# Performance work log

Hardware: AMD Instinct MI355X
Metric: run time of the kernel (lower is better)

Reference implementation:

```python
import jax, jax.numpy as jnp
import numpy as np
from jax import lax

DIM = 48
HEADS = 8
NBLK = 4
DN = ('NCHW', 'OIHW', 'NCHW')
EPS = 1e-12  # F.normalize clamp_min


def _to_blocks(t, b, heads, c, h1, w1, N):
    # 'b (head c) (h1 N_h) (w1 N_w) -> b head (c N_h N_w) (h1 w1)'
    t = t.reshape(b, heads, c, h1, N, w1, N)
    t = t.transpose(0, 1, 2, 4, 6, 3, 5)  # b head c N_h N_w h1 w1
    return t.reshape(b, heads, c * N * N, h1 * w1)


def _from_blocks(t, b, heads, c, h1, w1, N):
    t = t.reshape(b, heads, c, N, N, h1, w1)
    t = t.transpose(0, 1, 2, 5, 3, 6, 4)  # b head c h1 N_h w1 N_w
    return t.reshape(b, heads * c, h1 * N, w1 * N)


def setup_inputs() -> dict:
    key = jax.random.key(0)
    ks = jax.random.split(key, 5)
    return {
        'x': jax.random.normal(ks[0], (2, DIM, 512, 512), dtype=jnp.float32),
        'qkv_w': jax.random.normal(ks[1], (3 * DIM, DIM, 1, 1), dtype=jnp.float32) * 0.05,
        'dw_w': jax.random.normal(ks[2], (3 * DIM, 1, 3, 3), dtype=jnp.float32) * 0.05,
        'proj_w': jax.random.normal(ks[3], (DIM, DIM, 1, 1), dtype=jnp.float32) * 0.05,
        'temperature': jnp.ones((HEADS, 1, 1), dtype=jnp.float32),
    }


def reference(x, qkv_w, dw_w, proj_w, temperature):
    b, _, h, w = x.shape
    N = NBLK
    h_pad = (-h) % N
    w_pad = (-w) % N
    if h_pad or w_pad:
        x = jnp.pad(x, ((0, 0), (0, 0), (0, h_pad), (0, w_pad)), mode='reflect')
    h_after, w_after = h + h_pad, w + w_pad
    h1, w1 = h_after // N, w_after // N

    # 1x1 pointwise conv then 3x3 depthwise conv
    qkv = lax.conv_general_dilated(x, qkv_w, (1, 1), 'VALID', dimension_numbers=DN)
    qkv = lax.conv_general_dilated(qkv, dw_w, (1, 1), ((1, 1), (1, 1)),
                                   dimension_numbers=DN, feature_group_count=3 * DIM)
    q, k, v = jnp.split(qkv, 3, axis=1)

    c = DIM // HEADS
    q = _to_blocks(q, b, HEADS, c, h1, w1, N)  # [b, head, c*N*N, h1*w1]
    k = _to_blocks(k, b, HEADS, c, h1, w1, N)
    v = _to_blocks(v, b, HEADS, c, h1, w1, N)

    q = q / jnp.maximum(jnp.linalg.norm(q, axis=-1, keepdims=True), EPS)
    k = k / jnp.maximum(jnp.linalg.norm(k, axis=-1, keepdims=True), EPS)

    attn = jnp.einsum('bhcn,bhdn->bhcd', q, k) * temperature  # [b, head, cb, cb]
    attn = jax.nn.softmax(attn, axis=-1)
    out = jnp.einsum('bhcd,bhdn->bhcn', attn, v)

    out = _from_blocks(out, b, HEADS, c, h1, w1, N)  # [b, dim, h_after, w_after]
    out = lax.conv_general_dilated(out, proj_w, (1, 1), 'VALID', dimension_numbers=DN)
    return out[:, :, :h, :w]
```

## Files before the change

### kernel.cpp

```cpp
#include <hip/hip_runtime.h>
#include <cstddef>

#define S 512
#define SHIFT_HW 18
#define NCOL 16384

#define QB_OFF 0ull
#define KB_OFF 25165824ull
#define VB_OFF 50331648ull
#define G_OFF  75497472ull
#define SQ_OFF 75644928ull
#define SK_OFF 75646464ull
#define A_OFF  75648000ull

#define QS_STRIDE 327

__global__ __launch_bounds__(384, 4) void k1_qkv_dw(
    const float* __restrict__ x, const float* __restrict__ qkv_w,
    const float* __restrict__ dw_w,
    float* __restrict__ qb, float* __restrict__ kb, float* __restrict__ vb)
{
  const int t = threadIdx.x;
  const int b = blockIdx.z;
  const int W0 = blockIdx.x * 16, H0 = blockIdx.y * 16;
  __shared__ float qs[24 * QS_STRIDE];
  __shared__ float dws[1296];
  __shared__ float qws[2][1152];

  for (int i = t; i < 1296; i += 384) dws[i] = dw_w[i];
  for (int i = t; i < 288; i += 384)
    ((float4*)qws[0])[i] = ((const float4*)qkv_w)[i];

  float xv[48];
  const int p  = t;
  const int hy = p / 18, hx = p % 18;
  const int Hg = H0 - 1 + hy, Wg = W0 - 1 + hx;
  const bool inb = (t < 324) && (Hg >= 0) && (Hg < S) && (Wg >= 0) && (Wg < S);
  const float* xb = x + ((size_t)b * 48 << SHIFT_HW) + (inb ? ((Hg << 9) + Wg) : 0);
  #pragma unroll
  for (int ic = 0; ic < 48; ++ic) {
    float v = 0.0f;
    if (inb) v = xb[(size_t)ic << SHIFT_HW];
    xv[ic] = v;
  }

  const int ch = t >> 4;
  const int y  = t & 15;
  const int nb = (blockIdx.y * 4 + (y >> 2)) * 128 + blockIdx.x * 4;
  const float* qrow = qs + ch * QS_STRIDE + y * 18;

  __syncthreads();

  #pragma unroll 1
  for (int g = 0; g < 6; ++g) {
    if (t < 324) {
      const float* wgp = qws[g & 1];
      #pragma unroll
      for (int oc = 0; oc < 24; oc += 2) {
        float a0 = 0.f, a1 = 0.f;
        #pragma unroll
        for (int ic4 = 0; ic4 < 12; ++ic4) {
          const float4 w0 = *(const float4*)(wgp + oc * 48 + ic4 * 4);
          const float4 w1 = *(const float4*)(wgp + (oc + 1) * 48 + ic4 * 4);
          a0 += w0.x * xv[ic4 * 4 + 0] + w0.y * xv[ic4 * 4 + 1]
              + w0.z * xv[ic4 * 4 + 2] + w0.w * xv[ic4 * 4 + 3];
          a1 += w1.x * xv[ic4 * 4 + 0] + w1.y * xv[ic4 * 4 + 1]
              + w1.z * xv[ic4 * 4 + 2] + w1.w * xv[ic4 * 4 + 3];
        }
        qs[oc * QS_STRIDE + p]       = a0;
        qs[(oc + 1) * QS_STRIDE + p] = a1;
      }
    } else if (g < 5) {
      float4* dstq = (float4*)qws[(g + 1) & 1];
      const float4* srcq = (const float4*)qkv_w + (g + 1) * 288;
      for (int i = t - 324; i < 288; i += 60) dstq[i] = srcq[i];
    }
    __syncthreads();

    const int tensor = g >> 1;
    const int chbase = (g & 1) * 24;
    const int chg  = chbase + ch;
    const int head = chg / 6, c = chg - 6 * head;
    float* dst = (tensor == 0) ? qb : (tensor == 1) ? kb : vb;
    float* dstp = dst + (size_t)((b * 8 + head) * 16384 + nb) * 96
                      + c * 16 + (y & 3) * 4;
    const float* wp = dws + (tensor * 48 + chg) * 9;
    const float w0 = wp[0], w1 = wp[1], w2 = wp[2];
    const float w3 = wp[3], w4 = wp[4], w5 = wp[5];
    const float w6 = wp[6], w7 = wp[7], w8 = wp[8];

    float p00 = qrow[0], p01 = qrow[18], p02 = qrow[36];
    float p10 = qrow[1], p11 = qrow[19], p12 = qrow[37];
    #pragma unroll
    for (int wl = 0; wl < 4; ++wl) {
      float o[4];
      #pragma unroll
      for (int u = 0; u < 4; ++u) {
        const int xq = wl * 4 + u;
        const float n0 = qrow[xq + 2];
        const float n1 = qrow[xq + 20];
        const float n2 = qrow[xq + 38];
        o[u] = w0 * p00 + w1 * p10 + w2 * n0
             + w3 * p01 + w4 * p11 + w5 * n1
             + w6 * p02 + w7 * p12 + w8 * n2;
        p00 = p10; p01 = p11; p02 = p12;
        p10 = n0;  p11 = n1;  p12 = n2;
      }
      float4 v4 = {o[0], o[1], o[2], o[3]};
      *(float4*)(dstp + (size_t)wl * 96) = v4;
    }
    __syncthreads();
  }
}

__global__ __launch_bounds__(256, 3) void k3_gram(
    const float* __restrict__ qb, const float* __restrict__ kb,
    float* __restrict__ G, float* __restrict__ sq, float* __restrict__ sk)
{
  const int t  = threadIdx.x;
  const int bh = blockIdx.y;
  const int n0 = blockIdx.x * 256;
  __shared__ float qt[6144];
  __shared__ float kt[6144];
  const int ti = t >> 4, tj = t & 15;
  float acc[6][6];
  #pragma unroll
  for (int r = 0; r < 6; ++r)
    #pragma unroll
    for (int s_ = 0; s_ < 6; ++s_) acc[r][s_] = 0.f;
  float ss = 0.f;
  const float* qbase = qb + (size_t)bh * 16384 * 96;
  const float* kbase = kb + (size_t)bh * 16384 * 96;

  #pragma unroll 1
  for (int st = 0; st < 4; ++st) {
    __syncthreads();
    const float4* qsrc = (const float4*)(qbase + (size_t)(n0 + st * 64) * 96);
    const float4* ksrc = (const float4*)(kbase + (size_t)(n0 + st * 64) * 96);
    #pragma unroll
    for (int r = 0; r < 6; ++r) {
      const int f4 = r * 256 + t;
      ((float4*)qt)[f4] = qsrc[f4];
      ((float4*)kt)[f4] = ksrc[f4];
    }
    __syncthreads();
    #pragma unroll 2
    for (int nn = 0; nn < 64; ++nn) {
      const float* qr = qt + nn * 96 + ti * 6;
      const float* kr = kt + nn * 96 + tj * 6;
      const float2 q0 = *(const float2*)(qr);
      const float2 q1 = *(const float2*)(qr + 2);
      const float2 q2 = *(const float2*)(qr + 4);
      const float2 k0 = *(const float2*)(kr);
      const float2 k1 = *(const float2*)(kr + 2);
      const float2 k2 = *(const float2*)(kr + 4);
      const float qv[6] = {q0.x, q0.y, q1.x, q1.y, q2.x, q2.y};
      const float kv[6] = {k0.x, k0.y, k1.x, k1.y, k2.x, k2.y};
      #pragma unroll
      for (int r = 0; r < 6; ++r)
        #pragma unroll
        for (int s_ = 0; s_ < 6; ++s_)
          acc[r][s_] += qv[r] * kv[s_];
    }
    if (t < 192) {
      const float* base = (t < 96) ? qt : kt;
      const int srow = (t < 96) ? t : (t - 96);
      float s2 = 0.f;
      #pragma unroll 8
      for (int nn = 0; nn < 64; ++nn) {
        const float v = base[nn * 96 + srow];
        s2 += v * v;
      }
      ss += s2;
    }
  }
  float* Gb = G + (size_t)bh * 9216;
  #pragma unroll
  for (int r = 0; r < 6; ++r)
    #pragma unroll
    for (int s_ = 0; s_ < 6; ++s_)
      atomicAdd(Gb + (ti * 6 + r) * 96 + (tj * 6 + s_), acc[r][s_]);
  if (t < 96)       atomicAdd(sq + bh * 96 + t,        ss);
  else if (t < 192) atomicAdd(sk + bh * 96 + (t - 96), ss);
}

__global__ __launch_bounds__(128) void k4_softmax(
    const float* __restrict__ G, const float* __restrict__ sq,
    const float* __restrict__ sk, const float* __restrict__ temp,
    float* __restrict__ A)
{
  const int i  = blockIdx.x;
  const int bh = blockIdx.y;
  const int h  = bh & 7;
  const int t  = threadIdx.x;
  __shared__ float red[128];

  const float nq    = fmaxf(sqrtf(sq[bh * 96 + i]), 1e-12f);
  const float scale = temp[h] / nq;
  float logit = 0.f, val = -1e30f;
  if (t < 96) {
    const float nk = fmaxf(sqrtf(sk[bh * 96 + t]), 1e-12f);
    logit = G[(size_t)bh * 9216 + i * 96 + t] * scale / nk;
    val = logit;
  }
  red[t] = val; __syncthreads();
  #pragma unroll
  for (int o = 64; o > 0; o >>= 1) {
    if (t < o) red[t] = fmaxf(red[t], red[t + o]);
    __syncthreads();
  }
  const float m = red[0]; __syncthreads();
  const float e = (t < 96) ? __expf(logit - m) : 0.f;
  red[t] = e; __syncthreads();
  #pragma unroll
  for (int o = 64; o > 0; o >>= 1) {
    if (t < o) red[t] += red[t + o];
    __syncthreads();
  }
  const float ssum = red[0];
  if (t < 96) A[(size_t)bh * 9216 + i * 96 + t] = e / ssum;
}

__global__ __launch_bounds__(256, 3) void k5_av_proj(
    const float* __restrict__ vb, const float* __restrict__ A,
    const float* __restrict__ pw, float* __restrict__ out)
{
  const int t  = threadIdx.x;
  const int wg = blockIdx.x, hh = blockIdx.y, b = blockIdx.z;
  const int n0 = hh * 128 + wg * 16;
  __shared__ float smem[12288];

  #pragma unroll
  for (int it = 0; it < 12; ++it) {
    const int i4  = it * 256 + t;
    const int h   = i4 / 384;
    const int q   = i4 - h * 384;
    const int r4g = q >> 6;
    const int rem = q & 63;
    const int nl  = rem >> 2;
    const int r4  = r4g * 4 + (rem & 3);
    const float4 v = *(const float4*)(vb
        + (size_t)((b * 8 + h) * 16384 + n0 + nl) * 96 + r4 * 4);
    float* dl = smem + (h * 96 + r4 * 4) * 16 + nl;
    dl[0] = v.x; dl[16] = v.y; dl[32] = v.z; dl[48] = v.w;
  }
  __syncthreads();

  float4 res[6][2];
  #pragma unroll 1
  for (int r = 0; r < 6; ++r) {
    const int task = r * 256 + t;
    const int n4 = task & 3;
    const int ip = (task >> 2) % 48;
    const int h  = task / 192;
    const int i0 = ip * 2;
    const float* arow0 = A + (size_t)((b * 8 + h) * 96 + i0) * 96;
    const float* arow1 = arow0 + 96;
    const float* vp = smem + h * 1536 + n4 * 4;
    float4 a0 = {0, 0, 0, 0}, a1 = {0, 0, 0, 0};
    #pragma unroll 2
    for (int j4 = 0; j4 < 24; ++j4) {
      const float4 w0 = *(const float4*)(arow0 + j4 * 4);
      const float4 w1 = *(const float4*)(arow1 + j4 * 4);
      const float4 v0 = *(const float4*)(vp + (j4 * 4 + 0) * 16);
      const float4 v1 = *(const float4*)(vp + (j4 * 4 + 1) * 16);
      const float4 v2 = *(const float4*)(vp + (j4 * 4 + 2) * 16);
      const float4 v3 = *(const float4*)(vp + (j4 * 4 + 3) * 16);
      a0.x += w0.x * v0.x + w0.y * v1.x + w0.z * v2.x + w0.w * v3.x;
      a0.y += w0.x * v0.y + w0.y * v1.y + w0.z * v2.y + w0.w * v3.y;
      a0.z += w0.x * v0.z + w0.y * v1.z + w0.z * v2.z + w0.w * v3.z;
      a0.w += w0.x * v0.w + w0.y * v1.w + w0.z * v2.w + w0.w * v3.w;
      a1.x += w1.x * v0.x + w1.y * v1.x + w1.z * v2.x + w1.w * v3.x;
      a1.y += w1.x * v0.y + w1.y * v1.y + w1.z * v2.y + w1.w * v3.y;
      a1.z += w1.x * v0.z + w1.y * v1.z + w1.z * v2.z + w1.w * v3.z;
      a1.w += w1.x * v0.w + w1.y * v1.w + w1.z * v2.w + w1.w * v3.w;
    }
    res[r][0] = a0; res[r][1] = a1;
  }
  __syncthreads();

  #pragma unroll
  for (int r = 0; r < 6; ++r) {
    const int task = r * 256 + t;
    const int n4 = task & 3;
    const int ip = (task >> 2) % 48;
    const int h  = task / 192;
    const int i0 = ip * 2, i1 = i0 + 1;
    *(float4*)(smem + ((h * 6 + (i0 >> 4)) * 16 + (i0 & 15)) * 16 + n4 * 4) = res[r][0];
    *(float4*)(smem + ((h * 6 + (i1 >> 4)) * 16 + (i1 & 15)) * 16 + n4 * 4) = res[r][1];
  }
  __syncthreads();

  const int xl = t & 63, ph = t >> 6;
  const int p  = ph * 4 + (xl & 3);
  const int wwl = xl >> 2;
  float sv[48];
  #pragma unroll
  for (int ic = 0; ic < 48; ++ic) sv[ic] = smem[(ic * 16 + p) * 16 + wwl];
  const int H = hh * 4 + ph;
  const int Wp = wg * 64 + xl;
  float* outp = out + ((size_t)b * 48 << SHIFT_HW) + (H << 9) + Wp;
  #pragma unroll 1
  for (int oc = 0; oc < 48; oc += 2) {
    float acc0 = 0.f, acc1 = 0.f;
    #pragma unroll
    for (int ic = 0; ic < 48; ++ic) {
      acc0 += pw[oc * 48 + ic]       * sv[ic];
      acc1 += pw[(oc + 1) * 48 + ic] * sv[ic];
    }
    outp[(size_t)oc << SHIFT_HW]       = acc0;
    outp[(size_t)(oc + 1) << SHIFT_HW] = acc1;
  }
}

extern "C" void kernel_launch(void* const* d_in, const int* in_sizes, int n_in,
                              void* d_out, int out_size, void* d_ws, size_t ws_size,
                              hipStream_t stream) {
  const float* x      = (const float*)d_in[0];
  const float* qkv_w  = (const float*)d_in[1];
  const float* dw_w   = (const float*)d_in[2];
  const float* proj_w = (const float*)d_in[3];
  const float* temp   = (const float*)d_in[4];
  float* ws = (float*)d_ws;
  float* qb = ws + QB_OFF;
  float* kb = ws + KB_OFF;
  float* vb = ws + VB_OFF;
  float* G  = ws + G_OFF;
  float* sq = ws + SQ_OFF;
  float* sk = ws + SK_OFF;
  float* A  = ws + A_OFF;

  hipMemsetAsync(G, 0, (size_t)(147456 + 3072) * sizeof(float), stream);

  k1_qkv_dw<<<dim3(32, 32, 2), 384, 0, stream>>>(x, qkv_w, dw_w, qb, kb, vb);
  k3_gram<<<dim3(64, 16), 256, 0, stream>>>(qb, kb, G, sq, sk);
  k4_softmax<<<dim3(96, 16), 128, 0, stream>>>(G, sq, sk, temp, A);
  k5_av_proj<<<dim3(8, 128, 2), 256, 0, stream>>>(vb, A, proj_w, (float*)d_out);
}
```

Measured before the change: 874.0 us.

## Restage qkv weights via registers, write partial Grams, retile AV/proj kernel

k1 now uses a single qkv weight buffer. The next group's weights are loaded into registers during the depthwise stage and stored to shared memory afterwards, and occupancy and the smem stride are changed. k3 handles twice as many columns per block and writes per-block partial Gram matrices into the output buffer instead of using atomics, and k4 sums those 32 partials. k5 moves to 384 threads with an XCD-aware block index mapping, gives each thread full rows for the AV product, and adds a rotated smem layout to reduce bank conflicts. This trades atomic contention and the G memset for extra partial-sum reads in the softmax kernel.

```diff
diff --git a/kernel.cpp b/kernel.cpp
--- a/kernel.cpp
+++ b/kernel.cpp
@@ -8,14 +8,13 @@
 #define QB_OFF 0ull
 #define KB_OFF 25165824ull
 #define VB_OFF 50331648ull
-#define G_OFF  75497472ull
 #define SQ_OFF 75644928ull
 #define SK_OFF 75646464ull
 #define A_OFF  75648000ull
 
-#define QS_STRIDE 327
-
-__global__ __launch_bounds__(384, 4) void k1_qkv_dw(
+#define QS_STRIDE 324
+
+__global__ __launch_bounds__(384, 6) void k1_qkv_dw(
     const float* __restrict__ x, const float* __restrict__ qkv_w,
     const float* __restrict__ dw_w,
     float* __restrict__ qb, float* __restrict__ kb, float* __restrict__ vb)
@@ -25,11 +24,11 @@
   const int W0 = blockIdx.x * 16, H0 = blockIdx.y * 16;
   __shared__ float qs[24 * QS_STRIDE];
   __shared__ float dws[1296];
-  __shared__ float qws[2][1152];
+  __shared__ float qws[1152];
 
   for (int i = t; i < 1296; i += 384) dws[i] = dw_w[i];
   for (int i = t; i < 288; i += 384)
-    ((float4*)qws[0])[i] = ((const float4*)qkv_w)[i];
+    ((float4*)qws)[i] = ((const float4*)qkv_w)[i];
 
   float xv[48];
   const int p  = t;
@@ -54,7 +53,7 @@
   #pragma unroll 1
   for (int g = 0; g < 6; ++g) {
     if (t < 324) {
-      const float* wgp = qws[g & 1];
+      const float* wgp = qws;
       #pragma unroll
       for (int oc = 0; oc < 24; oc += 2) {
         float a0 = 0.f, a1 = 0.f;
@@ -70,12 +69,12 @@
         qs[oc * QS_STRIDE + p]       = a0;
         qs[(oc + 1) * QS_STRIDE + p] = a1;
       }
-    } else if (g < 5) {
-      float4* dstq = (float4*)qws[(g + 1) & 1];
-      const float4* srcq = (const float4*)qkv_w + (g + 1) * 288;
-      for (int i = t - 324; i < 288; i += 60) dstq[i] = srcq[i];
-    }
-    __syncthreads();
+    }
+    __syncthreads();
+
+    float4 stg;
+    const bool do_stage = (g < 5) && (t < 288);
+    if (do_stage) stg = *((const float4*)qkv_w + (g + 1) * 288 + t);
 
     const int tensor = g >> 1;
     const int chbase = (g & 1) * 24;
@@ -109,17 +108,19 @@
       float4 v4 = {o[0], o[1], o[2], o[3]};
       *(float4*)(dstp + (size_t)wl * 96) = v4;
     }
+
+    if (do_stage) ((float4*)qws)[t] = stg;
     __syncthreads();
   }
 }
 
 __global__ __launch_bounds__(256, 3) void k3_gram(
     const float* __restrict__ qb, const float* __restrict__ kb,
-    float* __restrict__ G, float* __restrict__ sq, float* __restrict__ sk)
+    float* __restrict__ Gp, float* __restrict__ sq, float* __restrict__ sk)
 {
   const int t  = threadIdx.x;
   const int bh = blockIdx.y;
-  const int n0 = blockIdx.x * 256;
+  const int n0 = blockIdx.x * 512;
   __shared__ float qt[6144];
   __shared__ float kt[6144];
   const int ti = t >> 4, tj = t & 15;
@@ -133,7 +134,7 @@
   const float* kbase = kb + (size_t)bh * 16384 * 96;
 
   #pragma unroll 1
-  for (int st = 0; st < 4; ++st) {
+  for (int st = 0; st < 8; ++st) {
     __syncthreads();
     const float4* qsrc = (const float4*)(qbase + (size_t)(n0 + st * 64) * 96);
     const float4* ksrc = (const float4*)(kbase + (size_t)(n0 + st * 64) * 96);
@@ -174,18 +175,18 @@
       ss += s2;
     }
   }
-  float* Gb = G + (size_t)bh * 9216;
+  float* Gb = Gp + (size_t)(blockIdx.x * 16 + bh) * 9216;
   #pragma unroll
   for (int r = 0; r < 6; ++r)
     #pragma unroll
     for (int s_ = 0; s_ < 6; ++s_)
-      atomicAdd(Gb + (ti * 6 + r) * 96 + (tj * 6 + s_), acc[r][s_]);
+      Gb[(ti * 6 + r) * 96 + (tj * 6 + s_)] = acc[r][s_];
   if (t < 96)       atomicAdd(sq + bh * 96 + t,        ss);
   else if (t < 192) atomicAdd(sk + bh * 96 + (t - 96), ss);
 }
 
 __global__ __launch_bounds__(128) void k4_softmax(
-    const float* __restrict__ G, const float* __restrict__ sq,
+    const float* __restrict__ Gp, const float* __restrict__ sq,
     const float* __restrict__ sk, const float* __restrict__ temp,
     float* __restrict__ A)
 {
@@ -199,8 +200,12 @@
   const float scale = temp[h] / nq;
   float logit = 0.f, val = -1e30f;
   if (t < 96) {
+    float gsum = 0.f;
+    #pragma unroll 8
+    for (int p = 0; p < 32; ++p)
+      gsum += Gp[(size_t)(p * 16 + bh) * 9216 + i * 96 + t];
     const float nk = fmaxf(sqrtf(sk[bh * 96 + t]), 1e-12f);
-    logit = G[(size_t)bh * 9216 + i * 96 + t] * scale / nk;
+    logit = gsum * scale / nk;
     val = logit;
   }
   red[t] = val; __syncthreads();
@@ -221,18 +226,22 @@
   if (t < 96) A[(size_t)bh * 9216 + i * 96 + t] = e / ssum;
 }
 
-__global__ __launch_bounds__(256, 3) void k5_av_proj(
+__global__ __launch_bounds__(384, 4) void k5_av_proj(
     const float* __restrict__ vb, const float* __restrict__ A,
     const float* __restrict__ pw, float* __restrict__ out)
 {
   const int t  = threadIdx.x;
-  const int wg = blockIdx.x, hh = blockIdx.y, b = blockIdx.z;
+  const int flat = blockIdx.x;
+  const int xcd  = flat & 7;
+  const int b    = xcd >> 2;
+  const int idx  = (xcd & 3) * 256 + (flat >> 3);
+  const int wg   = idx & 7, hh = idx >> 3;
   const int n0 = hh * 128 + wg * 16;
   __shared__ float smem[12288];
 
   #pragma unroll
-  for (int it = 0; it < 12; ++it) {
-    const int i4  = it * 256 + t;
+  for (int it = 0; it < 8; ++it) {
+    const int i4  = it * 384 + t;
     const int h   = i4 / 384;
     const int q   = i4 - h * 384;
     const int r4g = q >> 6;
@@ -246,70 +255,79 @@
   }
   __syncthreads();
 
-  float4 res[6][2];
-  #pragma unroll 1
-  for (int r = 0; r < 6; ++r) {
-    const int task = r * 256 + t;
-    const int n4 = task & 3;
-    const int ip = (task >> 2) % 48;
-    const int h  = task / 192;
-    const int i0 = ip * 2;
-    const float* arow0 = A + (size_t)((b * 8 + h) * 96 + i0) * 96;
-    const float* arow1 = arow0 + 96;
-    const float* vp = smem + h * 1536 + n4 * 4;
-    float4 a0 = {0, 0, 0, 0}, a1 = {0, 0, 0, 0};
-    #pragma unroll 2
-    for (int j4 = 0; j4 < 24; ++j4) {
-      const float4 w0 = *(const float4*)(arow0 + j4 * 4);
-      const float4 w1 = *(const float4*)(arow1 + j4 * 4);
-      const float4 v0 = *(const float4*)(vp + (j4 * 4 + 0) * 16);
-      const float4 v1 = *(const float4*)(vp + (j4 * 4 + 1) * 16);
-      const float4 v2 = *(const float4*)(vp + (j4 * 4 + 2) * 16);
-      const float4 v3 = *(const float4*)(vp + (j4 * 4 + 3) * 16);
-      a0.x += w0.x * v0.x + w0.y * v1.x + w0.z * v2.x + w0.w * v3.x;
-      a0.y += w0.x * v0.y + w0.y * v1.y + w0.z * v2.y + w0.w * v3.y;
-      a0.z += w0.x * v0.z + w0.y * v1.z + w0.z * v2.z + w0.w * v3.z;
-      a0.w += w0.x * v0.w + w0.y * v1.w + w0.z * v2.w + w0.w * v3.w;
-      a1.x += w1.x * v0.x + w1.y * v1.x + w1.z * v2.x + w1.w * v3.x;
-      a1.y += w1.x * v0.y + w1.y * v1.y + w1.z * v2.y + w1.w * v3.y;
-      a1.z += w1.x * v0.z + w1.y * v1.z + w1.z * v2.z + w1.w * v3.z;
-      a1.w += w1.x * v0.w + w1.y * v1.w + w1.z * v2.w + w1.w * v3.w;
-    }
-    res[r][0] = a0; res[r][1] = a1;
+  const int h  = t / 48;
+  const int ip = t - h * 48;
+  const int i0 = ip * 2;
+  const float* arow0 = A + (size_t)((b * 8 + h) * 96 + i0) * 96;
+  const float* arow1 = arow0 + 96;
+  const float* vbase = smem + h * 1536;
+  float4 r0[4], r1[4];
+  #pragma unroll
+  for (int n4 = 0; n4 < 4; ++n4) {
+    r0[n4] = float4{0, 0, 0, 0};
+    r1[n4] = float4{0, 0, 0, 0};
+  }
+  #pragma unroll 2
+  for (int j4 = 0; j4 < 24; ++j4) {
+    const float4 w0 = *(const float4*)(arow0 + j4 * 4);
+    const float4 w1 = *(const float4*)(arow1 + j4 * 4);
+    const float w0a[4] = {w0.x, w0.y, w0.z, w0.w};
+    const float w1a[4] = {w1.x, w1.y, w1.z, w1.w};
+    #pragma unroll
+    for (int u = 0; u < 4; ++u) {
+      const float* vp = vbase + (j4 * 4 + u) * 16;
+      const float wu0 = w0a[u], wu1 = w1a[u];
+      #pragma unroll
+      for (int n4 = 0; n4 < 4; ++n4) {
+        const float4 vv = *(const float4*)(vp + n4 * 4);
+        r0[n4].x += wu0 * vv.x; r0[n4].y += wu0 * vv.y;
+        r0[n4].z += wu0 * vv.z; r0[n4].w += wu0 * vv.w;
+        r1[n4].x += wu1 * vv.x; r1[n4].y += wu1 * vv.y;
+        r1[n4].z += wu1 * vv.z; r1[n4].w += wu1 * vv.w;
+      }
+    }
   }
   __syncthreads();
 
-  #pragma unroll
-  for (int r = 0; r < 6; ++r) {
-    const int task = r * 256 + t;
-    const int n4 = task & 3;
-    const int ip = (task >> 2) % 48;
-    const int h  = task / 192;
-    const int i0 = ip * 2, i1 = i0 + 1;
-    *(float4*)(smem + ((h * 6 + (i0 >> 4)) * 16 + (i0 & 15)) * 16 + n4 * 4) = res[r][0];
-    *(float4*)(smem + ((h * 6 + (i1 >> 4)) * 16 + (i1 & 15)) * 16 + n4 * 4) = res[r][1];
+  {
+    const int ic0 = h * 6 + (i0 >> 4);
+    const int p0w = i0 & 15;
+    const int i1 = i0 + 1;
+    const int ic1 = h * 6 + (i1 >> 4);
+    const int p1w = i1 & 15;
+    #pragma unroll
+    for (int n4 = 0; n4 < 4; ++n4) {
+      const int q0 = (n4 + (p0w >> 1)) & 3;
+      const int q1 = (n4 + (p1w >> 1)) & 3;
+      *(float4*)(smem + ic0 * 256 + p0w * 16 + q0 * 4) = r0[n4];
+      *(float4*)(smem + ic1 * 256 + p1w * 16 + q1 * 4) = r1[n4];
+    }
   }
   __syncthreads();
 
-  const int xl = t & 63, ph = t >> 6;
-  const int p  = ph * 4 + (xl & 3);
-  const int wwl = xl >> 2;
-  float sv[48];
-  #pragma unroll
-  for (int ic = 0; ic < 48; ++ic) sv[ic] = smem[(ic * 16 + p) * 16 + wwl];
-  const int H = hh * 4 + ph;
-  const int Wp = wg * 64 + xl;
-  float* outp = out + ((size_t)b * 48 << SHIFT_HW) + (H << 9) + Wp;
-  #pragma unroll 1
-  for (int oc = 0; oc < 48; oc += 2) {
-    float acc0 = 0.f, acc1 = 0.f;
-    #pragma unroll
-    for (int ic = 0; ic < 48; ++ic) {
-      acc0 += pw[oc * 48 + ic]       * sv[ic];
-      acc1 += pw[(oc + 1) * 48 + ic] * sv[ic];
-    }
-    outp[(size_t)oc << SHIFT_HW]       = acc0;
-    outp[(size_t)(oc + 1) << SHIFT_HW] = acc1;
+  if (t < 256) {
+    const int xl = t & 63, ph = t >> 6;
+    const int p  = ph * 4 + (xl & 3);
+    const int wwl = xl >> 2;
+    const int qp = ((wwl >> 2) + (p >> 1)) & 3;
+    const int wwp = qp * 4 + (wwl & 3);
+    float sv[48];
+    #pragma unroll
+    for (int ic = 0; ic < 48; ++ic) sv[ic] = smem[ic * 256 + p * 16 + wwp];
+    const int H = hh * 4 + ph;
+    const int Wp = wg * 64 + xl;
+    float* outp = out + ((size_t)b * 48 << SHIFT_HW) + (H << 9) + Wp;
+    #pragma unroll 1
+    for (int oc = 0; oc < 48; oc += 2) {
+      float acc0 = 0.f, acc1 = 0.f;
+      #pragma unroll
+      for (int ic = 0; ic < 48; ++ic) {
+        acc0 += pw[oc * 48 + ic]       * sv[ic];
+        acc1 += pw[(oc + 1) * 48 + ic] * sv[ic];
+      }
+      outp[(size_t)oc << SHIFT_HW]       = acc0;
+      outp[(size_t)(oc + 1) << SHIFT_HW] = acc1;
+    }
   }
 }
 
@@ -325,15 +343,15 @@
   float* qb = ws + QB_OFF;
   float* kb = ws + KB_OFF;
   float* vb = ws + VB_OFF;
-  float* G  = ws + G_OFF;
   float* sq = ws + SQ_OFF;
   float* sk = ws + SK_OFF;
   float* A  = ws + A_OFF;
-
-  hipMemsetAsync(G, 0, (size_t)(147456 + 3072) * sizeof(float), stream);
+  float* Gp = (float*)d_out;
+
+  hipMemsetAsync(sq, 0, (size_t)3072 * sizeof(float), stream);
 
   k1_qkv_dw<<<dim3(32, 32, 2), 384, 0, stream>>>(x, qkv_w, dw_w, qb, kb, vb);
-  k3_gram<<<dim3(64, 16), 256, 0, stream>>>(qb, kb, G, sq, sk);
-  k4_softmax<<<dim3(96, 16), 128, 0, stream>>>(G, sq, sk, temp, A);
-  k5_av_proj<<<dim3(8, 128, 2), 256, 0, stream>>>(vb, A, proj_w, (float*)d_out);
-}
+  k3_gram<<<dim3(32, 16), 256, 0, stream>>>(qb, kb, Gp, sq, sk);
+  k4_softmax<<<dim3(96, 16), 128, 0, stream>>>(Gp, sq, sk, temp, A);
+  k5_av_proj<<<2048, 384, 0, stream>>>(vb, A, proj_w, (float*)d_out);
+}
```

After: 719.7 us. 1.21x faster.
